# Kernel tuning notes

Hardware: AMD Instinct MI355X
Metric: run time of the kernel (lower is better)

## Reference

```python
import jax, jax.numpy as jnp
import numpy as np

TEMPERATURE = 0.07
MARGIN = 0.2
EPS = 1e-8  # matches torch F.cosine_similarity eps


def _cosine_matrix(a, b):
    # a: (N, D), b: (M, D) -> (N, M) pairwise cosine similarity
    an = a / jnp.clip(jnp.linalg.norm(a, axis=-1, keepdims=True), EPS)
    bn = b / jnp.clip(jnp.linalg.norm(b, axis=-1, keepdims=True), EPS)
    return an @ bn.T


def setup_inputs() -> dict:
    key = jax.random.key(0)
    k1, k2, k3 = jax.random.split(key, 3)
    return {
        "step_embeddings": jax.random.normal(k1, (8192, 1024), dtype=jnp.float32),
        "modal_embeddings": jax.random.normal(k2, (4096, 1024), dtype=jnp.float32),
        "negative_modal_embeddings": jax.random.normal(k3, (4096, 1024), dtype=jnp.float32),
    }


def reference(step_embeddings, modal_embeddings, negative_modal_embeddings):
    # --- step-modal alignment (max cosine sim per step, averaged) ---
    S = _cosine_matrix(step_embeddings, modal_embeddings)        # (N, M)
    per_step = S.max(axis=1)                                      # (N,)
    alignment = per_step.mean()

    # --- attention-weighted alignment (use_attention=True) ---
    logits = (step_embeddings @ modal_embeddings.T) / TEMPERATURE  # (N, M)
    attention = jax.nn.softmax(logits, axis=1)
    weighted_alignment = (S * attention).sum(axis=1).mean()

    # --- contrastive coherence against negatives ---
    Sn = _cosine_matrix(step_embeddings, negative_modal_embeddings)
    negative_alignment = Sn.max(axis=1).mean()
    positive_alignment = alignment
    contrastive_score = positive_alignment - negative_alignment
    margin_score = jax.nn.relu(contrastive_score - MARGIN)

    # --- per-step coherence (same max-cosine per step) ---
    min_step_coherence = per_step.min()

    # overall uses weighted_alignment (attention on), mixed with contrastive
    overall = 0.7 * weighted_alignment + 0.3 * contrastive_score

    return (alignment, weighted_alignment, attention, contrastive_score,
            margin_score, positive_alignment, negative_alignment,
            per_step, min_step_coherence, overall)
```

## Files before the change

### kernel.cpp

```cpp
#include <hip/hip_runtime.h>
#include <cmath>


#define WAVE 64

typedef __bf16 bf16x8_t __attribute__((ext_vector_type(8)));
typedef __bf16 bf16x4_t __attribute__((ext_vector_type(4)));
typedef float f32x4_t __attribute__((ext_vector_type(4)));

__device__ __forceinline__ float wave_reduce_sum(float v) {
#pragma unroll
    for (int o = 32; o > 0; o >>= 1) v += __shfl_down(v, o, WAVE);
    return v;
}
__device__ __forceinline__ float wave_reduce_max(float v) {
#pragma unroll
    for (int o = 32; o > 0; o >>= 1) v = fmaxf(v, __shfl_down(v, o, WAVE));
    return v;
}
__device__ __forceinline__ float wave_reduce_min(float v) {
#pragma unroll
    for (int o = 32; o > 0; o >>= 1) v = fminf(v, __shfl_down(v, o, WAVE));
    return v;
}

__device__ __forceinline__ unsigned enc_f(float f) {
    unsigned u = __float_as_uint(f);
    return (u & 0x80000000u) ? ~u : (u | 0x80000000u);
}
__device__ __forceinline__ float dec_f(unsigned e) {
    unsigned u = (e & 0x80000000u) ? (e & 0x7fffffffu) : ~e;
    return __uint_as_float(u);
}

__global__ __launch_bounds__(256)
void convert_norms_kernel(const float* __restrict__ step,
                          const float* __restrict__ modal,
                          const float* __restrict__ negs,
                          char* __restrict__ arena,
                          float* __restrict__ ina, float* __restrict__ inb,
                          float* __restrict__ inn,
                          unsigned* __restrict__ negmax_u, int N, int M) {
    const int tid = threadIdx.x, lane = tid & 63, wv = tid >> 6;
    const int b = blockIdx.x * 4 + wv;
    const float* src;
    if (b < N)          src = step  + (size_t)b * 1024;
    else if (b < N + M) src = modal + (size_t)(b - N) * 1024;
    else                src = negs  + (size_t)(b - N - M) * 1024;

    char* cb = arena + (((size_t)(b >> 2)) << 14) + ((size_t)(b & 3) << 11) + 8192;
    float s = 0.0f;
#pragma unroll
    for (int q = 0; q < 4; q++) {
        const int idx = lane + q * 64;
        const float4 v = ((const float4*)src)[idx];
        bf16x4_t o;
        o[0] = (__bf16)v.x; o[1] = (__bf16)v.y;
        o[2] = (__bf16)v.z; o[3] = (__bf16)v.w;
        *(bf16x4_t*)(cb + (size_t)idx * 8) = o;
        s += v.x * v.x + v.y * v.y + v.z * v.z + v.w * v.w;
    }
    s = wave_reduce_sum(s);
    if (lane == 0) {
        const float inv = 1.0f / fmaxf(sqrtf(s), 1e-8f);
        if (b < N)          { ina[b] = inv; negmax_u[b] = 0u; }
        else if (b < N + M) inb[b - N] = inv;
        else                inn[b - N - M] = inv;
    }
}

#define GLD16(g, l)                                                       \
    __builtin_amdgcn_global_load_lds(                                     \
        (const __attribute__((address_space(1))) void*)(g),               \
        (__attribute__((address_space(3))) void*)(l), 16, 0, 0)

#define BAR()   asm volatile("s_barrier" ::: "memory")
#define LGKM0() asm volatile("s_waitcnt lgkmcnt(0)" ::: "memory")
#define VMW(n)  asm volatile("s_waitcnt vmcnt(" #n ")" ::: "memory")

#define STAGE_A(Ab, kt)                                                   \
    _Pragma("unroll")                                                     \
    for (int h = 0; h < 2; h++)                                           \
    _Pragma("unroll")                                                     \
      for (int c = 0; c < 2; c++)                                         \
        GLD16(arena + srcA[h][c] + (size_t)(kt) * 128,                    \
              (Ab) + h * 8192 + c * 4096 + w * 512);

#define STAGE_B(Bb, kt)                                                   \
    _Pragma("unroll")                                                     \
    for (int h = 0; h < 2; h++)                                           \
    _Pragma("unroll")                                                     \
      for (int c = 0; c < 2; c++)                                         \
        GLD16(arena + srcB[h][c] + (size_t)(kt) * 128,                    \
              (Bb) + h * 8192 + c * 4096 + w * 512);

#define READ_A(g, Ab)                                                     \
    _Pragma("unroll")                                                     \
    for (int ii = 0; ii < 4; ii++)                                        \
    _Pragma("unroll")                                                     \
      for (int kk = 0; kk < 2; kk++)                                      \
        af[ii][kk] = *(const bf16x8_t*)&(Ab)[arow0 + (g) * 4096 +         \
                                             ii * 1024 + koff[kk]];

#define READ_B(j0, dst, Bb)                                               \
    _Pragma("unroll")                                                     \
    for (int jj = 0; jj < 2; jj++)                                        \
    _Pragma("unroll")                                                     \
      for (int kk = 0; kk < 2; kk++)                                      \
        dst[jj][kk] = *(const bf16x8_t*)&(Bb)[brow0 + ((j0) + jj) * 1024 +\
                                              koff[kk]];

#define MFMA_Q(i0, j0, bsrc)                                              \
    __builtin_amdgcn_s_setprio(1);                                        \
    _Pragma("unroll")                                                     \
    for (int kk = 0; kk < 2; kk++)                                        \
    _Pragma("unroll")                                                     \
      for (int ii = 0; ii < 4; ii++)                                      \
      _Pragma("unroll")                                                   \
        for (int jj = 0; jj < 2; jj++)                                    \
          acc[(i0) + ii][(j0) + jj] =                                     \
              __builtin_amdgcn_mfma_f32_16x16x32_bf16(                    \
                  af[ii][kk], bsrc[jj][kk], acc[(i0) + ii][(j0) + jj],    \
                  0, 0, 0);                                               \
    __builtin_amdgcn_s_setprio(0);

#define TILE(Ab, Bb, ktpre, pre)                                          \
                                                             \
    READ_A(0, Ab);                                                        \
    READ_B(0, bf01, Bb);                                                  \
    BAR(); LGKM0();                                                       \
    MFMA_Q(0, 0, bf01);                                                   \
    BAR();                                                                \
                                                             \
    READ_B(2, bf23, Bb);                                                  \
    BAR(); LGKM0();                                                       \
    MFMA_Q(0, 2, bf23);                                                   \
    BAR();                                                                \
     \
    READ_A(1, Ab);                                                        \
    if (pre) { STAGE_B(Bb, ktpre); }                                      \
    BAR(); LGKM0();                                                       \
    MFMA_Q(4, 0, bf01);                                                   \
    BAR();                                                                \
     \
    if (pre) { STAGE_A(Ab, ktpre); }                                      \
    BAR();                                                                \
    MFMA_Q(4, 2, bf23);                                                   \
    if (pre) { VMW(8); } else { VMW(0); }                                 \
    BAR();

__global__ __launch_bounds__(512, 2)
void gemm_fused_kernel(char* __restrict__ arena, int N, int M,
                       const float* __restrict__ inv_nn,
                       unsigned* __restrict__ negmax_u) {
    __shared__ __bf16 As[2][256 * 64];
    __shared__ __bf16 Bs[2][256 * 64];

    const int lin = blockIdx.x;
    const int xcd = lin & 7;
    const int j   = lin >> 3;
    const int r   = j >> 5;
    const int u   = j & 31;
    const int bm = ((xcd << 2) + (u & 3)) << 8;
    const int bn = ((r << 3) + (u >> 2)) << 8;

    const int t = threadIdx.x, w = t >> 6, lane = t & 63;
    const int lane16 = lane & 15, lq = lane >> 4;
    const int wm = w >> 2, wn = w & 3;

    const int l3 = lane >> 3, ol = lane & 7;
    const int og = ol ^ l3;
    unsigned srcA[2][2], srcB[2][2];
#pragma unroll
    for (int h = 0; h < 2; h++)
#pragma unroll
      for (int c = 0; c < 2; c++) {
        const int ga = bm + h * 128 + c * 64 + w * 8 + l3;
        srcA[h][c] = ((unsigned)(ga >> 2) << 14) + ((unsigned)(ga & 3) << 11)
                     + 8192u + (unsigned)og * 16u;
        const int gb = N + bn + h * 128 + c * 64 + w * 8 + l3;
        srcB[h][c] = ((unsigned)(gb >> 2) << 14) + ((unsigned)(gb & 3) << 11)
                     + 8192u + (unsigned)og * 16u;
      }

    const int sxr = lane16 & 7;
    int koff[2];
#pragma unroll
    for (int kk = 0; kk < 2; kk++) koff[kk] = ((lq + 4 * kk) ^ sxr) * 8;
    const int arow0 = wm * 8192 + lane16 * 64;
    const int brow0 = wn * 4096 + lane16 * 64;

    f32x4_t acc[8][4];
#pragma unroll
    for (int i = 0; i < 8; i++)
#pragma unroll
      for (int j2 = 0; j2 < 4; j2++) acc[i][j2] = (f32x4_t){0.f, 0.f, 0.f, 0.f};

    bf16x8_t af[4][2], bf01[2][2], bf23[2][2];

    __bf16* const A0 = As[0]; __bf16* const A1 = As[1];
    __bf16* const B0 = Bs[0]; __bf16* const B1 = Bs[1];

    STAGE_A(A0, 0); STAGE_B(B0, 0);
    STAGE_A(A1, 1); STAGE_B(B1, 1);
    VMW(8);
    BAR();

    for (int it = 0; it < 8; ++it) {
        const int pre = (it < 7);
        const int k2 = 2 * it + 2, k3 = 2 * it + 3;
        TILE(A0, B0, k2, pre)
        TILE(A1, B1, k3, pre)
    }

    if (bn < M) {
#pragma unroll
        for (int i = 0; i < 8; i++) {
#pragma unroll
            for (int rr = 0; rr < 4; rr++) {
                const int grow = bm + wm * 128 + i * 16 + lq * 4 + rr;
                __bf16* dst = (__bf16*)(arena + ((size_t)grow << 14)) +
                              bn + wn * 64 + lane16;
#pragma unroll
                for (int jj = 0; jj < 4; jj++)
                    dst[jj * 16] = (__bf16)acc[i][jj][rr];
            }
        }
    } else {
        float invn[4];
#pragma unroll
        for (int jj = 0; jj < 4; jj++)
            invn[jj] = inv_nn[(bn - M) + wn * 64 + jj * 16 + lane16];
#pragma unroll
        for (int i = 0; i < 8; i++) {
#pragma unroll
            for (int rr = 0; rr < 4; rr++) {
                float v = acc[i][0][rr] * invn[0];
                v = fmaxf(v, acc[i][1][rr] * invn[1]);
                v = fmaxf(v, acc[i][2][rr] * invn[2]);
                v = fmaxf(v, acc[i][3][rr] * invn[3]);
#pragma unroll
                for (int o = 8; o > 0; o >>= 1)
                    v = fmaxf(v, __shfl_xor(v, o, WAVE));
                if (lane16 == 0)
                    atomicMax(&negmax_u[bm + wm * 128 + i * 16 + lq * 4 + rr],
                              enc_f(v));
            }
        }
    }
}

#define CUT 2.0f
#define MAXCAND 64

__global__ __launch_bounds__(256)
void softmax_fix_kernel(char* __restrict__ arena, const float* __restrict__ step,
                        const float* __restrict__ modal,
                        const float* __restrict__ ina, const float* __restrict__ inb,
                        float* __restrict__ perstep, float* __restrict__ wout,
                        float* __restrict__ attn) {
    const int row = blockIdx.x, tid = threadIdx.x;
    const int lane = tid & 63, wv = tid >> 6;

    __shared__ float srow_s[1024];
    __shared__ float red[8];
    __shared__ float bcast[2];
    __shared__ int   cand[MAXCAND];
    __shared__ float exact[MAXCAND];
    __shared__ int   cnt;

    if (tid == 0) cnt = 0;
    ((float4*)srow_s)[tid] = ((const float4*)(step + (size_t)row * 1024))[tid];

    const __bf16* gb = (const __bf16*)(arena + ((size_t)row << 14));
    float vals[16];
    float invn[16];
#pragma unroll
    for (int g = 0; g < 4; g++) {
        const bf16x4_t v = *(const bf16x4_t*)(gb + g * 1024 + tid * 4);
        const float4 x = *(const float4*)(inb + g * 1024 + tid * 4);
        vals[g * 4 + 0] = (float)v[0]; vals[g * 4 + 1] = (float)v[1];
        vals[g * 4 + 2] = (float)v[2]; vals[g * 4 + 3] = (float)v[3];
        invn[g * 4 + 0] = x.x; invn[g * 4 + 1] = x.y;
        invn[g * 4 + 2] = x.z; invn[g * 4 + 3] = x.w;
    }

    float dmax = -3.4e38f;
#pragma unroll
    for (int j = 0; j < 16; j++) dmax = fmaxf(dmax, vals[j]);
    float wm = wave_reduce_max(dmax);
    if (lane == 0) red[wv] = wm;
    __syncthreads();
    if (tid == 0) bcast[0] = fmaxf(fmaxf(red[0], red[1]), fmaxf(red[2], red[3]));
    __syncthreads();
    const float m0 = bcast[0];

    const float thr = m0 - CUT;
#pragma unroll
    for (int g = 0; g < 4; g++)
#pragma unroll
        for (int u = 0; u < 4; u++) {
            if (vals[g * 4 + u] >= thr) {
                const int pos = atomicAdd(&cnt, 1);
                if (pos < MAXCAND) cand[pos] = g * 1024 + tid * 4 + u;
            }
        }
    __syncthreads();
    const int nc = min(cnt, MAXCAND);

    for (int i = wv; i < nc; i += 4) {
        const float* mrow = modal + (size_t)cand[i] * 1024;
        float p = 0.0f;
#pragma unroll
        for (int q = 0; q < 16; q++) {
            const int idx = lane + q * 64;
            p = fmaf(srow_s[idx], mrow[idx], p);
        }
        p = wave_reduce_sum(p);
        if (lane == 0) exact[i] = p;
    }
    __syncthreads();

    for (int i = 0; i < nc; i++) {
        const int c = cand[i];
        if (((c & 1023) >> 2) == tid) vals[(c >> 10) * 4 + (c & 3)] = exact[i];
    }

    float dmax2 = -3.4e38f, cmax = -3.4e38f;
#pragma unroll
    for (int j = 0; j < 16; j++) {
        dmax2 = fmaxf(dmax2, vals[j]);
        cmax = fmaxf(cmax, vals[j] * invn[j]);
    }
    float wg = wave_reduce_max(dmax2);
    float wc = wave_reduce_max(cmax);
    if (lane == 0) { red[wv] = wg; red[4 + wv] = wc; }
    __syncthreads();
    if (tid == 0) {
        bcast[0] = fmaxf(fmaxf(red[0], red[1]), fmaxf(red[2], red[3]));
        bcast[1] = fmaxf(fmaxf(red[4], red[5]), fmaxf(red[6], red[7]));
    }
    __syncthreads();
    const float invT = 1.0f / 0.07f;
    const float mlog = bcast[0] * invT;
    const float cmaxAll = bcast[1];

    float evals[16];
    float lsum = 0.0f;
#pragma unroll
    for (int j = 0; j < 16; j++) {
        const float e = __expf(vals[j] * invT - mlog);
        evals[j] = e;
        lsum += e;
    }
    lsum = wave_reduce_sum(lsum);
    __syncthreads();
    if (lane == 0) red[wv] = lsum;
    __syncthreads();
    if (tid == 0) bcast[0] = red[0] + red[1] + red[2] + red[3];
    __syncthreads();
    const float invZ = 1.0f / bcast[0];

    float* arow = attn + (size_t)row * 4096;
    float wacc = 0.0f;
#pragma unroll
    for (int g = 0; g < 4; g++) {
        float4 o;
        const float a0 = evals[g * 4 + 0] * invZ, a1 = evals[g * 4 + 1] * invZ;
        const float a2 = evals[g * 4 + 2] * invZ, a3 = evals[g * 4 + 3] * invZ;
        o.x = a0; o.y = a1; o.z = a2; o.w = a3;
        *(float4*)(arow + g * 1024 + tid * 4) = o;
        wacc += a0 * vals[g * 4 + 0] * invn[g * 4 + 0];
        wacc += a1 * vals[g * 4 + 1] * invn[g * 4 + 1];
        wacc += a2 * vals[g * 4 + 2] * invn[g * 4 + 2];
        wacc += a3 * vals[g * 4 + 3] * invn[g * 4 + 3];
    }
    wacc = wave_reduce_sum(wacc);
    __syncthreads();
    if (lane == 0) red[wv] = wacc;
    __syncthreads();
    if (tid == 0) {
        const float inv_na = ina[row];
        perstep[row] = cmaxAll * inv_na;
        wout[row] = (red[0] + red[1] + red[2] + red[3]) * inv_na;
    }
}

__global__ __launch_bounds__(1024)
void finalize_kernel(const float* __restrict__ perstep, const float* __restrict__ w,
                     const unsigned* __restrict__ negmax_u,
                     const float* __restrict__ ina, float* __restrict__ out,
                     int N, size_t NM) {
    float s_a = 0.0f, s_w = 0.0f, s_n = 0.0f, mn = 3.4e38f;
    for (int i = threadIdx.x; i < N; i += 1024) {
        const float p = perstep[i];
        s_a += p;
        s_w += w[i];
        s_n += dec_f(negmax_u[i]) * ina[i];
        mn = fminf(mn, p);
    }
    s_a = wave_reduce_sum(s_a);
    s_w = wave_reduce_sum(s_w);
    s_n = wave_reduce_sum(s_n);
    mn  = wave_reduce_min(mn);
    __shared__ float ra[16], rw[16], rn[16], rm[16];
    const int lane = threadIdx.x & 63, wv = threadIdx.x >> 6;
    if (lane == 0) { ra[wv] = s_a; rw[wv] = s_w; rn[wv] = s_n; rm[wv] = mn; }
    __syncthreads();
    if (threadIdx.x == 0) {
        float ta = 0, tw = 0, tn = 0, tm = 3.4e38f;
#pragma unroll
        for (int i = 0; i < 16; i++) {
            ta += ra[i]; tw += rw[i]; tn += rn[i]; tm = fminf(tm, rm[i]);
        }
        const float inv = 1.0f / (float)N;
        const float alignment = ta * inv;
        const float weighted  = tw * inv;
        const float neg       = tn * inv;
        const float contrast  = alignment - neg;
        const float margin    = fmaxf(contrast - 0.2f, 0.0f);
        const float overall   = 0.7f * weighted + 0.3f * contrast;
        out[0] = alignment;
        out[1] = weighted;
        float* p = out + 2 + NM;
        p[0] = contrast;
        p[1] = margin;
        p[2] = alignment;
        p[3] = neg;
        p[4 + N] = tm;
        p[5 + N] = overall;
    }
}

extern "C" void kernel_launch(void* const* d_in, const int* in_sizes, int n_in,
                              void* d_out, int out_size, void* d_ws, size_t ws_size,
                              hipStream_t stream) {
    const float* step  = (const float*)d_in[0];
    const float* modal = (const float*)d_in[1];
    const float* negs  = (const float*)d_in[2];
    float* out = (float*)d_out;

    const int K = 1024;
    const int N = in_sizes[0] / K;
    const int M = in_sizes[1] / K;
    const size_t NM = (size_t)N * (size_t)M;

    float* ina        = (float*)d_ws;
    float* inb        = ina + N;
    float* inn        = inb + M;
    unsigned* negmax  = (unsigned*)(inn + M);
    float* wsum       = (float*)(negmax + N);

    char* arena    = (char*)d_out + 16;
    float* attn    = out + 2;
    float* perstep = out + 2 + NM + 4;

    convert_norms_kernel<<<(N + 2 * M) / 4, 256, 0, stream>>>(
        step, modal, negs, arena, ina, inb, inn, negmax, N, M);

    const int nblocks = (N >> 8) * ((2 * M) >> 8);
    gemm_fused_kernel<<<nblocks, 512, 0, stream>>>(arena, N, M, inn, negmax);

    softmax_fix_kernel<<<N, 256, 0, stream>>>(arena, step, modal, ina, inb,
                                              perstep, wsum, attn);

    finalize_kernel<<<1, 1024, 0, stream>>>(perstep, wsum, negmax, ina, out, N, NM);
}
```

Before: 360.9 us.

## Prefetch next tile's LDS fragments and trim barriers in GEMM main loop

Restructures the double-buffered GEMM tile macro so the first A and B fragments of the next LDS buffer are read at the end of the current tile. The MFMA block of the next tile can then start without waiting on a fresh LDS read. The number of workgroup barriers per tile drops from seven to at most three, which cuts synchronisation stalls between waves. The cost is extra register pressure, and the correctness of the write-after-read ordering now rests on the fewer remaining barriers.

```diff
diff --git a/kernel.cpp b/kernel.cpp
--- a/kernel.cpp
+++ b/kernel.cpp
@@ -110,6 +110,9 @@
         dst[jj][kk] = *(const bf16x8_t*)&(Bb)[brow0 + ((j0) + jj) * 1024 +\
                                               koff[kk]];
 
+#define READ_B01(Bb) READ_B(0, bf01, Bb)
+#define READ_B23(Bb) READ_B(2, bf23, Bb)
+
 #define MFMA_Q(i0, j0, bsrc)                                              \
     __builtin_amdgcn_s_setprio(1);                                        \
     _Pragma("unroll")                                                     \
@@ -124,30 +127,26 @@
                   0, 0, 0);                                               \
     __builtin_amdgcn_s_setprio(0);
 
-#define TILE(Ab, Bb, ktpre, pre)                                          \
-                                                             \
-    READ_A(0, Ab);                                                        \
-    READ_B(0, bf01, Bb);                                                  \
-    BAR(); LGKM0();                                                       \
+#define TILE(Ac, Bc, An, Bn, ktpre, pre, rd)                              \
+    LGKM0();                     \
     MFMA_Q(0, 0, bf01);                                                   \
-    BAR();                                                                \
-                                                             \
-    READ_B(2, bf23, Bb);                                                  \
-    BAR(); LGKM0();                                                       \
+    READ_B23(Bc);                           \
+    LGKM0();                                                              \
     MFMA_Q(0, 2, bf23);                                                   \
-    BAR();                                                                \
-     \
-    READ_A(1, Ab);                                                        \
-    if (pre) { STAGE_B(Bb, ktpre); }                                      \
-    BAR(); LGKM0();                                                       \
+    READ_A(1, Ac);          \
+    BAR();                        \
+    if (pre) { STAGE_B(Bc, ktpre); }                                      \
+    LGKM0();                                             \
     MFMA_Q(4, 0, bf01);                                                   \
-    BAR();                                                                \
-     \
-    if (pre) { STAGE_A(Ab, ktpre); }                                      \
-    BAR();                                                                \
+    BAR();                        \
+    if (pre) { STAGE_A(Ac, ktpre); }                                      \
     MFMA_Q(4, 2, bf23);                                                   \
-    if (pre) { VMW(8); } else { VMW(0); }                                 \
-    BAR();
+    if (rd) {                                                             \
+        if (pre) { VMW(8); } else { VMW(0); }                             \
+        BAR();                      \
+        READ_A(0, An);           \
+        READ_B01(Bn);                                                     \
+    }
 
 __global__ __launch_bounds__(512, 2)
 void gemm_fused_kernel(char* __restrict__ arena, int N, int M,
@@ -205,12 +204,14 @@
     STAGE_A(A1, 1); STAGE_B(B1, 1);
     VMW(8);
     BAR();
+    READ_A(0, A0);
+    READ_B01(B0);
 
     for (int it = 0; it < 8; ++it) {
         const int pre = (it < 7);
         const int k2 = 2 * it + 2, k3 = 2 * it + 3;
-        TILE(A0, B0, k2, pre)
-        TILE(A1, B1, k3, pre)
+        TILE(A0, B0, A1, B1, k2, pre, 1)
+        TILE(A1, B1, A0, B0, k3, pre, pre)
     }
 
     if (bn < M) {
```

Result: faster. 353.2 us (-2.1%).
